# Performance work log

Hardware: AMD Instinct MI355X
Metric: run time of the kernel (lower is better)

Reference implementation:

```python
import jax, jax.numpy as jnp
import numpy as np

B, S, DQK, DV, H = 4, 2048, 128, 128, 8


def setup_inputs() -> dict:
    key = jax.random.key(0)
    ks = jax.random.split(key, 9)
    s = 0.02
    return {
        "query": jax.random.normal(ks[0], (B, S, DQK), jnp.float32),
        "key": jax.random.normal(ks[1], (B, S, DQK), jnp.float32),
        "value": jax.random.normal(ks[2], (B, S, DV), jnp.float32),
        "WQ": jax.random.normal(ks[3], (DQK, H * DQK), jnp.float32) * s,
        "bQ": jax.random.normal(ks[4], (H * DQK,), jnp.float32) * s,
        "WK": jax.random.normal(ks[5], (DQK, H * DQK), jnp.float32) * s,
        "bK": jax.random.normal(ks[6], (H * DQK,), jnp.float32) * s,
        "WV": jax.random.normal(ks[7], (DV, H * DV), jnp.float32) * s,
        "bV": jax.random.normal(ks[8], (H * DV,), jnp.float32) * s,
    }


def reference(query, key, value, WQ, bQ, WK, bK, WV, bV):
    b, qn, dqk = query.shape
    kn = key.shape[1]
    dv = value.shape[2]
    h = H
    # projections -> [b, n, h, d]
    Q = (query @ WQ + bQ).reshape(b, qn, h, dqk)
    K = (key @ WK + bK).reshape(b, kn, h, dqk)
    V = (value @ WV + bV).reshape(b, kn, h, dv)
    # abs(QK^T)/sqrt(dk) score -- non-standard, prevents flash kernels
    scores = jnp.abs(jnp.einsum("bqhd,bkhd->bhqk", Q, K)) / jnp.sqrt(
        jnp.asarray(dqk, query.dtype)
    )
    w = jax.nn.softmax(scores, axis=-1)  # [b,h,q,k]
    # (complex cast +0j in the original is numerically a no-op on real V)
    out = jnp.einsum("bhqk,bkhd->bqhd", w, V).reshape(b, qn, h * dv)
    return out
```

## Files before the change

### kernel.cpp

```cpp
#include <hip/hip_runtime.h>
#include <hip/hip_bf16.h>

#define B_ 4
#define S_ 2048
#define D_ 128
#define H_ 8

typedef __attribute__((ext_vector_type(8))) short bf16x8;
typedef __attribute__((ext_vector_type(4))) float f32x4;

__device__ __forceinline__ short f2bf(float f) {
  union { float f; unsigned u; } v; v.f = f;
  unsigned u = v.u;
  unsigned r = (u + 0x7FFFu + ((u >> 16) & 1u)) >> 16;
  return (short)r;
}

__device__ __forceinline__ short4 pack4(f32x4 p) {
  union { __hip_bfloat162 h2[2]; short4 s4; } u;
  u.h2[0] = __float22bfloat162_rn(make_float2(p[0], p[1]));
  u.h2[1] = __float22bfloat162_rn(make_float2(p[2], p[3]));
  return u.s4;
}

__device__ __forceinline__ void dma16(const short* g, short* l) {
  __builtin_amdgcn_global_load_lds(
      (const __attribute__((address_space(1))) unsigned int*)g,
      (__attribute__((address_space(3))) unsigned int*)l, 16, 0, 0);
}

__global__ __launch_bounds__(256) void prep(
    const float* __restrict__ a, const float* __restrict__ b, const float* __restrict__ c,
    short* __restrict__ oa, short* __restrict__ ob, short* __restrict__ oc,
    const float* __restrict__ WQ, const float* __restrict__ WK, const float* __restrict__ WV,
    short* __restrict__ TQ, short* __restrict__ TK, short* __restrict__ TV) {
  __shared__ float tile[64][65];
  if (blockIdx.x < 3072) {
    int i = blockIdx.x * 256 + threadIdx.x;
    int which = i >> 18;
    int j = i & 262143;
    const float* in = (which == 0) ? a : (which == 1) ? b : c;
    short* out = (which == 0) ? oa : (which == 1) ? ob : oc;
    float4 v = ((const float4*)in)[j];
    short4 o = make_short4(f2bf(v.x), f2bf(v.y), f2bf(v.z), f2bf(v.w));
    ((short4*)out)[j] = o;
  } else {
    int bid = blockIdx.x - 3072;
    int bw = bid >> 5;
    int tl = bid & 31;
    int n0 = (tl & 15) * 64, k0 = (tl >> 4) * 64;
    const float* W = (bw == 0) ? WQ : (bw == 1) ? WK : WV;
    short* Wt = (bw == 0) ? TQ : (bw == 1) ? TK : TV;
#pragma unroll
    for (int i = 0; i < 16; ++i) {
      int cix = threadIdx.x + 256 * i;
      int rr = cix >> 6, cc = cix & 63;
      tile[rr][cc] = W[(k0 + rr) * 1024 + n0 + cc];
    }
    __syncthreads();
#pragma unroll
    for (int i = 0; i < 16; ++i) {
      int cix = threadIdx.x + 256 * i;
      int rr = cix >> 6, cc = cix & 63;
      Wt[(n0 + rr) * 128 + k0 + cc] = f2bf(tile[cc][rr]);
    }
  }
}

template <int WA>
__device__ __forceinline__ void proj_tile(const short* __restrict__ X,
                                          const short* __restrict__ Wt,
                                          const float* __restrict__ bias,
                                          short* __restrict__ out,
                                          int mtile, int ntile,
                                          short* sA, short* sB) {
  int tid = threadIdx.x;
  int lane = tid & 63, w = tid >> 6;
  int l15 = lane & 15, l4 = lane >> 4;
  int m0 = mtile * 128, n0 = ntile * 128;

#pragma unroll
  for (int j = 0; j < 8; ++j) {
    int f = w * 8 + j;
    const short* src = X + (m0 + (f >> 2) * 16 + l15) * 128 + (f & 3) * 32 + l4 * 8;
    dma16(src, sA + f * 512);
  }
#pragma unroll
  for (int j = 0; j < 8; ++j) {
    int f = w * 8 + j;
    const short* src = Wt + (n0 + (f >> 2) * 16 + l15) * 128 + (f & 3) * 32 + l4 * 8;
    dma16(src, sB + f * 512);
  }
  __syncthreads();

  int wr = w >> 1, wc = w & 1;
  f32x4 acc[4][4];
#pragma unroll
  for (int mi = 0; mi < 4; ++mi)
#pragma unroll
    for (int ni = 0; ni < 4; ++ni) acc[mi][ni] = (f32x4){0.f, 0.f, 0.f, 0.f};

#pragma unroll
  for (int mi = 0; mi < 4; ++mi) {
    bf16x8 a[4];
#pragma unroll
    for (int st = 0; st < 4; ++st)
      a[st] = *(const bf16x8*)(sA + ((wr * 4 + mi) * 4 + st) * 512 + lane * 8);
#pragma unroll
    for (int ni = 0; ni < 4; ++ni) {
#pragma unroll
      for (int st = 0; st < 4; ++st) {
        bf16x8 b = *(const bf16x8*)(sB + ((wc * 4 + ni) * 4 + st) * 512 + lane * 8);
        if (WA)
          acc[mi][ni] = __builtin_amdgcn_mfma_f32_16x16x32_bf16(b, a[st], acc[mi][ni], 0, 0, 0);
        else
          acc[mi][ni] = __builtin_amdgcn_mfma_f32_16x16x32_bf16(a[st], b, acc[mi][ni], 0, 0, 0);
      }
    }
  }

  if (WA) {
#pragma unroll
    for (int mi = 0; mi < 4; ++mi) {
      int sg = m0 + wr * 64 + mi * 16 + l15;
      int bb = sg >> 11, s = sg & 2047;
      short* orow = out + ((size_t)(bb * H_ + ntile) * S_ + s) * D_;
#pragma unroll
      for (int ni = 0; ni < 4; ++ni) {
        int d0 = wc * 64 + ni * 16 + l4 * 4;
        float4 bv = *(const float4*)(bias + n0 + d0);
        f32x4 t = acc[mi][ni];
        t[0] += bv.x; t[1] += bv.y; t[2] += bv.z; t[3] += bv.w;
        *(short4*)(orow + d0) = pack4(t);
      }
    }
  } else {
#pragma unroll
    for (int ni = 0; ni < 4; ++ni) {
      int d = wc * 64 + ni * 16 + l15;
      float bvs = bias[n0 + d];
#pragma unroll
      for (int mi = 0; mi < 4; ++mi) {
        int sg0 = m0 + wr * 64 + mi * 16 + l4 * 4;
        int bb = sg0 >> 11, s0 = sg0 & 2047;
        f32x4 t = acc[mi][ni];
        t[0] += bvs; t[1] += bvs; t[2] += bvs; t[3] += bvs;
        size_t off = (size_t)(bb * H_ + ntile) * (S_ * D_)
                   + (size_t)(s0 >> 6) * 8192
                   + (size_t)((d >> 4) * 2 + ((s0 >> 5) & 1)) * 512
                   + ((s0 >> 3) & 3) * 128 + (d & 15) * 8
                   + (s0 & 7);
        *(short4*)(out + off) = pack4(t);
      }
    }
  }
}

__global__ __launch_bounds__(256, 2) void proj3(
    const short* __restrict__ xq, const short* __restrict__ xk, const short* __restrict__ xv,
    const short* __restrict__ wtq, const short* __restrict__ wtk, const short* __restrict__ wtv,
    const float* __restrict__ bQ, const float* __restrict__ bK, const float* __restrict__ bV,
    short* __restrict__ Qp, short* __restrict__ Kp, short* __restrict__ Vf) {
  __shared__ short sA[16384], sB[16384];
  int work = (blockIdx.x & 7) * 192 + (blockIdx.x >> 3);
  int which = work >> 9;
  int t = work & 511;
  int mtile = t >> 3, ntile = t & 7;
  if (which == 0)      proj_tile<1>(xq, wtq, bQ, Qp, mtile, ntile, sA, sB);
  else if (which == 1) proj_tile<1>(xk, wtk, bK, Kp, mtile, ntile, sA, sB);
  else                 proj_tile<0>(xv, wtv, bV, Vf, mtile, ntile, sA, sB);
}

#define BN 64
#define PSTR 72

#define ATTN_ITER(KB, KN, IT)                                                  \
  {                                                                            \
    if ((IT) + 1 < S_ / BN) {                                                  \
      int kt_ = ((IT) + 1) * BN;                                               \
      const short* kgs = kg + kt_ * D_;                                        \
      short* kl = (KN) + (w * 4) * 512;                                        \
      dma16(kgs, kl);                                                          \
      dma16(kgs + 32, kl + 512);                                               \
      dma16(kgs + 64, kl + 1024);                                              \
      dma16(kgs + 96, kl + 1536);                                              \
    }                                                                          \
       \
    bf16x8 bv[16];                                                             \
    _Pragma("unroll") for (int f = 0; f < 8; ++f)                              \
      bv[f] = *(const bf16x8*)(vfb + (IT) * 8192 + f * 512);                   \
    __builtin_amdgcn_sched_barrier(0);                                         \
             \
    f32x4 s0[4], s1[4];                                                        \
    __builtin_amdgcn_s_setprio(1);                                             \
    _Pragma("unroll") for (int mt = 0; mt < 4; ++mt) {                         \
      s0[mt] = (f32x4){0.f, 0.f, 0.f, 0.f};                                    \
      s1[mt] = (f32x4){0.f, 0.f, 0.f, 0.f};                                    \
      _Pragma("unroll") for (int st = 0; st < 4; ++st) {                       \
        bf16x8 bk = *(const bf16x8*)((KB) + (mt * 4 + st) * 512 + lane * 8);   \
        s0[mt] = __builtin_amdgcn_mfma_f32_16x16x32_bf16(bk, aq[0][st], s0[mt], 0, 0, 0); \
        s1[mt] = __builtin_amdgcn_mfma_f32_16x16x32_bf16(bk, aq[1][st], s1[mt], 0, 0, 0); \
      }                                                                        \
    }                                                                          \
    __builtin_amdgcn_s_setprio(0);                                             \
         \
    _Pragma("unroll") for (int f = 8; f < 16; ++f)                             \
      bv[f] = *(const bf16x8*)(vfb + (IT) * 8192 + f * 512);                   \
    __builtin_amdgcn_sched_barrier(0);                                         \
     \
    bf16x8 ap0[2], ap1[2];                                                     \
    _Pragma("unroll") for (int mt = 0; mt < 4; ++mt) {                         \
      _Pragma("unroll") for (int r = 0; r < 4; ++r) {                          \
        float p = __builtin_amdgcn_exp2f(fabsf(s0[mt][r]) * SC2);              \
        ls0 += p;                                                              \
        s0[mt][r] = p;                                                         \
      }                                                                        \
      *(short4*)(pw + l15 * PSTR + mt * 16 + l4 * 4) = pack4(s0[mt]);          \
    }                                                                          \
    ap0[0] = *(const bf16x8*)(pw + l15 * PSTR + l4 * 8);                       \
    ap0[1] = *(const bf16x8*)(pw + l15 * PSTR + 32 + l4 * 8);                  \
                 \
    _Pragma("unroll") for (int mt = 0; mt < 4; ++mt) {                         \
      _Pragma("unroll") for (int r = 0; r < 4; ++r) {                          \
        float p = __builtin_amdgcn_exp2f(fabsf(s1[mt][r]) * SC2);              \
        ls1 += p;                                                              \
        s1[mt][r] = p;                                                         \
      }                                                                        \
      *(short4*)(pw + l15 * PSTR + mt * 16 + l4 * 4) = pack4(s1[mt]);          \
    }                                                                          \
    ap1[0] = *(const bf16x8*)(pw + l15 * PSTR + l4 * 8);                       \
    ap1[1] = *(const bf16x8*)(pw + l15 * PSTR + 32 + l4 * 8);                  \
                      \
    __builtin_amdgcn_s_setprio(1);                                             \
    _Pragma("unroll") for (int t = 0; t < 8; ++t) {                            \
      _Pragma("unroll") for (int kst = 0; kst < 2; ++kst) {                    \
        o0[t] = __builtin_amdgcn_mfma_f32_16x16x32_bf16(ap0[kst], bv[t * 2 + kst], o0[t], 0, 0, 0); \
        o1[t] = __builtin_amdgcn_mfma_f32_16x16x32_bf16(ap1[kst], bv[t * 2 + kst], o1[t], 0, 0, 0); \
      }                                                                        \
    }                                                                          \
    __builtin_amdgcn_s_setprio(0);                                             \
    __syncthreads();     \
  }

__global__ __launch_bounds__(256, 2) void attn(const short* __restrict__ Qp,
                                               const short* __restrict__ Kp,
                                               const short* __restrict__ Vf,
                                               float* __restrict__ out) {
  __shared__ short sK0[8192], sK1[8192];
  __shared__ short sP[4 * 16 * PSTR];

  int tid = threadIdx.x;
  int lane = tid & 63, w = tid >> 6;
  int swz = (blockIdx.x & 7) * 64 + (blockIdx.x >> 3);
  int qt = swz & 15;
  int bh = swz >> 4;
  int q0 = qt * 128;
  int l15 = lane & 15, l4 = lane >> 4;

  const short* Qbase = Qp + (size_t)bh * S_ * D_;
  const short* Kbase = Kp + (size_t)bh * S_ * D_;
  const short* vfb = Vf + (size_t)bh * S_ * D_ + lane * 8;

  const short* kg = Kbase + (w * 16 + l15) * D_ + l4 * 8;

  {
    short* kl = sK0 + (w * 4) * 512;
    dma16(kg, kl);
    dma16(kg + 32, kl + 512);
    dma16(kg + 64, kl + 1024);
    dma16(kg + 96, kl + 1536);
  }

  bf16x8 aq[2][4];
#pragma unroll
  for (int g = 0; g < 2; ++g)
#pragma unroll
    for (int st = 0; st < 4; ++st)
      aq[g][st] = *(const bf16x8*)(Qbase + (q0 + w * 32 + g * 16 + l15) * D_ + l4 * 8 + 32 * st);

  f32x4 o0[8], o1[8];
#pragma unroll
  for (int t = 0; t < 8; ++t) {
    o0[t] = (f32x4){0.f, 0.f, 0.f, 0.f};
    o1[t] = (f32x4){0.f, 0.f, 0.f, 0.f};
  }
  float ls0 = 0.f, ls1 = 0.f;

  const float SC2 = 0.127530637f;
  short* pw = sP + w * 16 * PSTR;

  __syncthreads();

  for (int it = 0; it < S_ / BN; it += 2) {
    ATTN_ITER(sK0, sK1, it);
    ATTN_ITER(sK1, sK0, it + 1);
  }

  ls0 += __shfl_xor(ls0, 16);
  ls0 += __shfl_xor(ls0, 32);
  ls1 += __shfl_xor(ls1, 16);
  ls1 += __shfl_xor(ls1, 32);
  float inv0[4], inv1[4];
#pragma unroll
  for (int r = 0; r < 4; ++r) {
    inv0[r] = 1.f / __shfl(ls0, l4 * 4 + r);
    inv1[r] = 1.f / __shfl(ls1, l4 * 4 + r);
  }

  int bb = bh >> 3, h = bh & 7;
#pragma unroll
  for (int t = 0; t < 8; ++t) {
#pragma unroll
    for (int r = 0; r < 4; ++r) {
      int qA = q0 + w * 32 + l4 * 4 + r;
      int qB = qA + 16;
      out[((size_t)(bb * S_ + qA)) * (H_ * D_) + h * D_ + t * 16 + l15] = o0[t][r] * inv0[r];
      out[((size_t)(bb * S_ + qB)) * (H_ * D_) + h * D_ + t * 16 + l15] = o1[t][r] * inv1[r];
    }
  }
}

extern "C" void kernel_launch(void* const* d_in, const int* in_sizes, int n_in,
                              void* d_out, int out_size, void* d_ws, size_t ws_size,
                              hipStream_t stream) {
  (void)in_sizes; (void)n_in; (void)out_size; (void)ws_size;
  const float* q  = (const float*)d_in[0];
  const float* k  = (const float*)d_in[1];
  const float* v  = (const float*)d_in[2];
  const float* WQ = (const float*)d_in[3];
  const float* bQ = (const float*)d_in[4];
  const float* WK = (const float*)d_in[5];
  const float* bK = (const float*)d_in[6];
  const float* WV = (const float*)d_in[7];
  const float* bV = (const float*)d_in[8];

  const int NX = B_ * S_ * D_;
  const int NW = D_ * H_ * D_;
  const int NP = B_ * H_ * S_ * D_;

  short* ws  = (short*)d_ws;
  short* xq  = ws;
  short* xk  = xq + NX;
  short* xv  = xk + NX;
  short* wtq = xv + NX;
  short* wtk = wtq + NW;
  short* wtv = wtk + NW;
  short* Qp  = wtv + NW;
  short* Kp  = Qp + NP;
  short* Vf  = Kp + NP;

  prep<<<3168, 256, 0, stream>>>(q, k, v, xq, xk, xv, WQ, WK, WV, wtq, wtk, wtv);

  proj3<<<1536, 256, 0, stream>>>(xq, xk, xv, wtq, wtk, wtv, bQ, bK, bV, Qp, Kp, Vf);

  attn<<<512, 256, 0, stream>>>(Qp, Kp, Vf, (float*)d_out);
}
```

Baseline: 193.2 us.

## Fuse input bf16 conversion into projection and software-pipeline attention softmax with PV

The fp32 activation-to-bf16 conversion is removed from the prep kernel. The projection kernel now loads fp32 inputs directly and converts them on the fly into LDS, which cuts a full read/write pass over the inputs. The attention loop is restructured so each iteration runs the QK MFMAs for tile t+1 and the PV MFMAs for tile t together, then does the softmax. This overlaps exp work with matrix work but adds a prologue/epilogue and keeps more values live in registers.

```diff
diff --git a/kernel.cpp b/kernel.cpp
--- a/kernel.cpp
+++ b/kernel.cpp
@@ -30,45 +30,31 @@
 }
 
 __global__ __launch_bounds__(256) void prep(
-    const float* __restrict__ a, const float* __restrict__ b, const float* __restrict__ c,
-    short* __restrict__ oa, short* __restrict__ ob, short* __restrict__ oc,
     const float* __restrict__ WQ, const float* __restrict__ WK, const float* __restrict__ WV,
     short* __restrict__ TQ, short* __restrict__ TK, short* __restrict__ TV) {
   __shared__ float tile[64][65];
-  if (blockIdx.x < 3072) {
-    int i = blockIdx.x * 256 + threadIdx.x;
-    int which = i >> 18;
-    int j = i & 262143;
-    const float* in = (which == 0) ? a : (which == 1) ? b : c;
-    short* out = (which == 0) ? oa : (which == 1) ? ob : oc;
-    float4 v = ((const float4*)in)[j];
-    short4 o = make_short4(f2bf(v.x), f2bf(v.y), f2bf(v.z), f2bf(v.w));
-    ((short4*)out)[j] = o;
-  } else {
-    int bid = blockIdx.x - 3072;
-    int bw = bid >> 5;
-    int tl = bid & 31;
-    int n0 = (tl & 15) * 64, k0 = (tl >> 4) * 64;
-    const float* W = (bw == 0) ? WQ : (bw == 1) ? WK : WV;
-    short* Wt = (bw == 0) ? TQ : (bw == 1) ? TK : TV;
-#pragma unroll
-    for (int i = 0; i < 16; ++i) {
-      int cix = threadIdx.x + 256 * i;
-      int rr = cix >> 6, cc = cix & 63;
-      tile[rr][cc] = W[(k0 + rr) * 1024 + n0 + cc];
-    }
-    __syncthreads();
-#pragma unroll
-    for (int i = 0; i < 16; ++i) {
-      int cix = threadIdx.x + 256 * i;
-      int rr = cix >> 6, cc = cix & 63;
-      Wt[(n0 + rr) * 128 + k0 + cc] = f2bf(tile[cc][rr]);
-    }
+  int bw = blockIdx.x >> 5;
+  int tl = blockIdx.x & 31;
+  int n0 = (tl & 15) * 64, k0 = (tl >> 4) * 64;
+  const float* W = (bw == 0) ? WQ : (bw == 1) ? WK : WV;
+  short* Wt = (bw == 0) ? TQ : (bw == 1) ? TK : TV;
+#pragma unroll
+  for (int i = 0; i < 16; ++i) {
+    int cix = threadIdx.x + 256 * i;
+    int rr = cix >> 6, cc = cix & 63;
+    tile[rr][cc] = W[(k0 + rr) * 1024 + n0 + cc];
+  }
+  __syncthreads();
+#pragma unroll
+  for (int i = 0; i < 16; ++i) {
+    int cix = threadIdx.x + 256 * i;
+    int rr = cix >> 6, cc = cix & 63;
+    Wt[(n0 + rr) * 128 + k0 + cc] = f2bf(tile[cc][rr]);
   }
 }
 
 template <int WA>
-__device__ __forceinline__ void proj_tile(const short* __restrict__ X,
+__device__ __forceinline__ void proj_tile(const float* __restrict__ X,
                                           const short* __restrict__ Wt,
                                           const float* __restrict__ bias,
                                           short* __restrict__ out,
@@ -82,14 +68,19 @@
 #pragma unroll
   for (int j = 0; j < 8; ++j) {
     int f = w * 8 + j;
-    const short* src = X + (m0 + (f >> 2) * 16 + l15) * 128 + (f & 3) * 32 + l4 * 8;
-    dma16(src, sA + f * 512);
+    const short* src = Wt + (n0 + (f >> 2) * 16 + l15) * 128 + (f & 3) * 32 + l4 * 8;
+    dma16(src, sB + f * 512);
   }
 #pragma unroll
   for (int j = 0; j < 8; ++j) {
     int f = w * 8 + j;
-    const short* src = Wt + (n0 + (f >> 2) * 16 + l15) * 128 + (f & 3) * 32 + l4 * 8;
-    dma16(src, sB + f * 512);
+    const float* src = X + (size_t)(m0 + (f >> 2) * 16 + l15) * 128 + (f & 3) * 32 + l4 * 8;
+    float4 v0 = *(const float4*)src;
+    float4 v1 = *(const float4*)(src + 4);
+    union { struct { short4 lo, hi; } s; bf16x8 v; } u;
+    u.s.lo = pack4((f32x4){v0.x, v0.y, v0.z, v0.w});
+    u.s.hi = pack4((f32x4){v1.x, v1.y, v1.z, v1.w});
+    *(bf16x8*)(sA + f * 512 + lane * 8) = u.v;
   }
   __syncthreads();
 
@@ -157,7 +148,7 @@
 }
 
 __global__ __launch_bounds__(256, 2) void proj3(
-    const short* __restrict__ xq, const short* __restrict__ xk, const short* __restrict__ xv,
+    const float* __restrict__ xq, const float* __restrict__ xk, const float* __restrict__ xv,
     const short* __restrict__ wtq, const short* __restrict__ wtk, const short* __restrict__ wtv,
     const float* __restrict__ bQ, const float* __restrict__ bK, const float* __restrict__ bV,
     short* __restrict__ Qp, short* __restrict__ Kp, short* __restrict__ Vf) {
@@ -174,72 +165,55 @@
 #define BN 64
 #define PSTR 72
 
-#define ATTN_ITER(KB, KN, IT)                                                  \
+#define KDMA(BUF, T)                                                           \
   {                                                                            \
-    if ((IT) + 1 < S_ / BN) {                                                  \
-      int kt_ = ((IT) + 1) * BN;                                               \
-      const short* kgs = kg + kt_ * D_;                                        \
-      short* kl = (KN) + (w * 4) * 512;                                        \
-      dma16(kgs, kl);                                                          \
-      dma16(kgs + 32, kl + 512);                                               \
-      dma16(kgs + 64, kl + 1024);                                              \
-      dma16(kgs + 96, kl + 1536);                                              \
+    const short* kgs = kg + (T) * BN * D_;                                     \
+    short* kl = (BUF) + (w * 4) * 512;                                         \
+    dma16(kgs, kl);                                                            \
+    dma16(kgs + 32, kl + 512);                                                 \
+    dma16(kgs + 64, kl + 1024);                                                \
+    dma16(kgs + 96, kl + 1536);                                                \
+  }
+
+#define QK_CLUSTER(KB)                                                         \
+  _Pragma("unroll") for (int mt = 0; mt < 4; ++mt) {                           \
+    s0[mt] = (f32x4){0.f, 0.f, 0.f, 0.f};                                      \
+    s1[mt] = (f32x4){0.f, 0.f, 0.f, 0.f};                                      \
+    _Pragma("unroll") for (int st = 0; st < 4; ++st) {                         \
+      bf16x8 bk = *(const bf16x8*)((KB) + (mt * 4 + st) * 512 + lane * 8);     \
+      s0[mt] = __builtin_amdgcn_mfma_f32_16x16x32_bf16(bk, aq[0][st], s0[mt], 0, 0, 0); \
+      s1[mt] = __builtin_amdgcn_mfma_f32_16x16x32_bf16(bk, aq[1][st], s1[mt], 0, 0, 0); \
     }                                                                          \
-       \
-    bf16x8 bv[16];                                                             \
-    _Pragma("unroll") for (int f = 0; f < 8; ++f)                              \
-      bv[f] = *(const bf16x8*)(vfb + (IT) * 8192 + f * 512);                   \
-    __builtin_amdgcn_sched_barrier(0);                                         \
-             \
-    f32x4 s0[4], s1[4];                                                        \
-    __builtin_amdgcn_s_setprio(1);                                             \
-    _Pragma("unroll") for (int mt = 0; mt < 4; ++mt) {                         \
-      s0[mt] = (f32x4){0.f, 0.f, 0.f, 0.f};                                    \
-      s1[mt] = (f32x4){0.f, 0.f, 0.f, 0.f};                                    \
-      _Pragma("unroll") for (int st = 0; st < 4; ++st) {                       \
-        bf16x8 bk = *(const bf16x8*)((KB) + (mt * 4 + st) * 512 + lane * 8);   \
-        s0[mt] = __builtin_amdgcn_mfma_f32_16x16x32_bf16(bk, aq[0][st], s0[mt], 0, 0, 0); \
-        s1[mt] = __builtin_amdgcn_mfma_f32_16x16x32_bf16(bk, aq[1][st], s1[mt], 0, 0, 0); \
-      }                                                                        \
+  }
+
+#define SM_CLUSTER()                                                           \
+  _Pragma("unroll") for (int mt = 0; mt < 4; ++mt) {                           \
+    _Pragma("unroll") for (int r = 0; r < 4; ++r) {                            \
+      float p = __builtin_amdgcn_exp2f(fabsf(s0[mt][r]) * SC2);                \
+      ls0 += p;                                                                \
+      s0[mt][r] = p;                                                           \
     }                                                                          \
-    __builtin_amdgcn_s_setprio(0);                                             \
-         \
-    _Pragma("unroll") for (int f = 8; f < 16; ++f)                             \
-      bv[f] = *(const bf16x8*)(vfb + (IT) * 8192 + f * 512);                   \
-    __builtin_amdgcn_sched_barrier(0);                                         \
-     \
-    bf16x8 ap0[2], ap1[2];                                                     \
-    _Pragma("unroll") for (int mt = 0; mt < 4; ++mt) {                         \
-      _Pragma("unroll") for (int r = 0; r < 4; ++r) {                          \
-        float p = __builtin_amdgcn_exp2f(fabsf(s0[mt][r]) * SC2);              \
-        ls0 += p;                                                              \
-        s0[mt][r] = p;                                                         \
-      }                                                                        \
-      *(short4*)(pw + l15 * PSTR + mt * 16 + l4 * 4) = pack4(s0[mt]);          \
+    *(short4*)(pw + l15 * PSTR + mt * 16 + l4 * 4) = pack4(s0[mt]);            \
+  }                                                                            \
+  ap0[0] = *(const bf16x8*)(pw + l15 * PSTR + l4 * 8);                         \
+  ap0[1] = *(const bf16x8*)(pw + l15 * PSTR + 32 + l4 * 8);                    \
+  _Pragma("unroll") for (int mt = 0; mt < 4; ++mt) {                           \
+    _Pragma("unroll") for (int r = 0; r < 4; ++r) {                            \
+      float p = __builtin_amdgcn_exp2f(fabsf(s1[mt][r]) * SC2);                \
+      ls1 += p;                                                                \
+      s1[mt][r] = p;                                                           \
     }                                                                          \
-    ap0[0] = *(const bf16x8*)(pw + l15 * PSTR + l4 * 8);                       \
-    ap0[1] = *(const bf16x8*)(pw + l15 * PSTR + 32 + l4 * 8);                  \
-                 \
-    _Pragma("unroll") for (int mt = 0; mt < 4; ++mt) {                         \
-      _Pragma("unroll") for (int r = 0; r < 4; ++r) {                          \
-        float p = __builtin_amdgcn_exp2f(fabsf(s1[mt][r]) * SC2);              \
-        ls1 += p;                                                              \
-        s1[mt][r] = p;                                                         \
-      }                                                                        \
-      *(short4*)(pw + l15 * PSTR + mt * 16 + l4 * 4) = pack4(s1[mt]);          \
+    *(short4*)(pw + l15 * PSTR + mt * 16 + l4 * 4) = pack4(s1[mt]);            \
+  }                                                                            \
+  ap1[0] = *(const bf16x8*)(pw + l15 * PSTR + l4 * 8);                         \
+  ap1[1] = *(const bf16x8*)(pw + l15 * PSTR + 32 + l4 * 8);
+
+#define PV_CLUSTER()                                                           \
+  _Pragma("unroll") for (int t8 = 0; t8 < 8; ++t8) {                           \
+    _Pragma("unroll") for (int kst = 0; kst < 2; ++kst) {                      \
+      o0[t8] = __builtin_amdgcn_mfma_f32_16x16x32_bf16(ap0[kst], bv[t8 * 2 + kst], o0[t8], 0, 0, 0); \
+      o1[t8] = __builtin_amdgcn_mfma_f32_16x16x32_bf16(ap1[kst], bv[t8 * 2 + kst], o1[t8], 0, 0, 0); \
     }                                                                          \
-    ap1[0] = *(const bf16x8*)(pw + l15 * PSTR + l4 * 8);                       \
-    ap1[1] = *(const bf16x8*)(pw + l15 * PSTR + 32 + l4 * 8);                  \
-                      \
-    __builtin_amdgcn_s_setprio(1);                                             \
-    _Pragma("unroll") for (int t = 0; t < 8; ++t) {                            \
-      _Pragma("unroll") for (int kst = 0; kst < 2; ++kst) {                    \
-        o0[t] = __builtin_amdgcn_mfma_f32_16x16x32_bf16(ap0[kst], bv[t * 2 + kst], o0[t], 0, 0, 0); \
-        o1[t] = __builtin_amdgcn_mfma_f32_16x16x32_bf16(ap1[kst], bv[t * 2 + kst], o1[t], 0, 0, 0); \
-      }                                                                        \
-    }                                                                          \
-    __builtin_amdgcn_s_setprio(0);                                             \
-    __syncthreads();     \
   }
 
 __global__ __launch_bounds__(256, 2) void attn(const short* __restrict__ Qp,
@@ -263,13 +237,7 @@
 
   const short* kg = Kbase + (w * 16 + l15) * D_ + l4 * 8;
 
-  {
-    short* kl = sK0 + (w * 4) * 512;
-    dma16(kg, kl);
-    dma16(kg + 32, kl + 512);
-    dma16(kg + 64, kl + 1024);
-    dma16(kg + 96, kl + 1536);
-  }
+  KDMA(sK0, 0);
 
   bf16x8 aq[2][4];
 #pragma unroll
@@ -291,9 +259,39 @@
 
   __syncthreads();
 
-  for (int it = 0; it < S_ / BN; it += 2) {
-    ATTN_ITER(sK0, sK1, it);
-    ATTN_ITER(sK1, sK0, it + 1);
+  f32x4 s0[4], s1[4];
+  bf16x8 ap0[2], ap1[2];
+
+  KDMA(sK1, 1);
+  QK_CLUSTER(sK0);
+  SM_CLUSTER();
+  __syncthreads();
+
+  for (int t = 0; t < 31; ++t) {
+    bf16x8 bv[16];
+#pragma unroll
+    for (int f = 0; f < 16; ++f)
+      bv[f] = *(const bf16x8*)(vfb + t * 8192 + f * 512);
+    __builtin_amdgcn_sched_barrier(0);
+    if (t < 30) {
+      short* kdst = (t & 1) ? sK1 : sK0;
+      KDMA(kdst, t + 2);
+    }
+    const short* kb = (t & 1) ? sK0 : sK1;
+    __builtin_amdgcn_s_setprio(1);
+    QK_CLUSTER(kb);
+    PV_CLUSTER();
+    __builtin_amdgcn_s_setprio(0);
+    SM_CLUSTER();
+    __syncthreads();
+  }
+
+  {
+    bf16x8 bv[16];
+#pragma unroll
+    for (int f = 0; f < 16; ++f)
+      bv[f] = *(const bf16x8*)(vfb + 31 * 8192 + f * 512);
+    PV_CLUSTER();
   }
 
   ls0 += __shfl_xor(ls0, 16);
@@ -334,24 +332,20 @@
   const float* WV = (const float*)d_in[7];
   const float* bV = (const float*)d_in[8];
 
-  const int NX = B_ * S_ * D_;
   const int NW = D_ * H_ * D_;
   const int NP = B_ * H_ * S_ * D_;
 
   short* ws  = (short*)d_ws;
-  short* xq  = ws;
-  short* xk  = xq + NX;
-  short* xv  = xk + NX;
-  short* wtq = xv + NX;
+  short* wtq = ws;
   short* wtk = wtq + NW;
   short* wtv = wtk + NW;
   short* Qp  = wtv + NW;
   short* Kp  = Qp + NP;
   short* Vf  = Kp + NP;
 
-  prep<<<3168, 256, 0, stream>>>(q, k, v, xq, xk, xv, WQ, WK, WV, wtq, wtk, wtv);
-
-  proj3<<<1536, 256, 0, stream>>>(xq, xk, xv, wtq, wtk, wtv, bQ, bK, bV, Qp, Kp, Vf);
+  prep<<<96, 256, 0, stream>>>(WQ, WK, WV, wtq, wtk, wtv);
+
+  proj3<<<1536, 256, 0, stream>>>(q, k, v, wtq, wtk, wtv, bQ, bK, bV, Qp, Kp, Vf);
 
   attn<<<512, 256, 0, stream>>>(Qp, Kp, Vf, (float*)d_out);
 }
```

Result: no change. 196.5 us (+1.7%).
